# Performance work log

Measured on AMD Instinct MI355X. Metric: run time of the kernel, lower is better.

The kernel has to match this reference:

```python
import jax, jax.numpy as jnp
import numpy as np

NUM_GROUPS = 32
EPS = 1e-05
HT_MIN = -1.0
HT_MAX = 1.0


def setup_inputs() -> dict:
    key = jax.random.key(0)
    k1, k2, k3 = jax.random.split(key, 3)
    B, IN, OUT = 4096, 2048, 2048
    x = jax.random.normal(k1, (B, IN), dtype=jnp.float32)
    # kaiming-uniform-ish scale for weight, uniform bias bound 1/sqrt(in)
    weight = jax.random.normal(k2, (OUT, IN), dtype=jnp.float32) * (1.0 / np.sqrt(IN))
    bias = jax.random.uniform(k3, (OUT,), dtype=jnp.float32, minval=-1.0 / np.sqrt(IN), maxval=1.0 / np.sqrt(IN))
    gn_weight = jnp.ones((OUT,), dtype=jnp.float32)
    gn_bias = jnp.zeros((OUT,), dtype=jnp.float32)
    return {"x": x, "weight": weight, "bias": bias, "gn_weight": gn_weight, "gn_bias": gn_bias}


def reference(x, weight, bias, gn_weight, gn_bias):
    # Linear: y = x @ W^T + b   -> [B, OUT]
    y = jnp.einsum("bi,oi->bo", x, weight) + bias
    B, C = y.shape
    G = NUM_GROUPS
    yg = y.reshape(B, G, C // G)
    mean = jnp.mean(yg, axis=-1, keepdims=True)
    var = jnp.mean(jnp.square(yg), axis=-1, keepdims=True) - jnp.square(mean)
    yn = ((yg - mean) * jax.lax.rsqrt(var + EPS)).reshape(B, C)
    out = yn * gn_weight + gn_bias
    return jnp.clip(out, HT_MIN, HT_MAX)
```

## Files before the change

kernel.cpp:

```cpp
#include <hip/hip_runtime.h>
#include <stdint.h>

#define B_ROWS 4096
#define C_OUT  2048
#define C_IN   2048
#define EPS    1e-5f

typedef __attribute__((ext_vector_type(8))) short bf16x8;
typedef __attribute__((ext_vector_type(4))) float f32x4;

__device__ __forceinline__ unsigned short f2bf(float f) {
    uint32_t u = __float_as_uint(f);
    uint32_t r = (u + 0x7fffu + ((u >> 16) & 1u)) >> 16;
    return (unsigned short)r;
}

__global__ void cvt_f32_bf16_kernel(const float* __restrict__ in,
                                    unsigned short* __restrict__ out, int n4) {
    int i = blockIdx.x * blockDim.x + threadIdx.x;
    if (i < n4) {
        float4 v = ((const float4*)in)[i];
        ushort4 o;
        o.x = f2bf(v.x); o.y = f2bf(v.y); o.z = f2bf(v.z); o.w = f2bf(v.w);
        ((ushort4*)out)[i] = o;
    }
}

__global__ void gemm_gn_kernel(const unsigned short* __restrict__ A,
                               const unsigned short* __restrict__ W,
                               const float* __restrict__ bias,
                               const float* __restrict__ gnw,
                               const float* __restrict__ gnb,
                               float* __restrict__ out) {
    __shared__ unsigned short sA[128 * 32];
    __shared__ unsigned short sB[128 * 32];

    const int bc   = blockIdx.x;
    const int br   = blockIdx.y;
    const int t    = threadIdx.x;
    const int lane = t & 63;
    const int wave = t >> 6;
    const int wr   = wave >> 1;
    const int wc   = wave & 1;
    const int c16  = lane & 15;
    const int quad = lane >> 4;

    f32x4 acc[4][4];
#pragma unroll
    for (int i = 0; i < 4; i++)
#pragma unroll
        for (int j = 0; j < 4; j++) acc[i][j] = (f32x4){0.f, 0.f, 0.f, 0.f};

    const int fl0 = t * 8;
    const int r0  = fl0 >> 5;
    const int kk0 = fl0 & 31;
    const unsigned short* gA = A + (size_t)(br * 128 + r0) * C_IN + kk0;
    const unsigned short* gB = W + (size_t)(bc * 128 + r0) * C_IN + kk0;

    for (int k0 = 0; k0 < C_IN; k0 += 32) {
        __builtin_amdgcn_global_load_lds(
            (const __attribute__((address_space(1))) void*)(gA + k0),
            (__attribute__((address_space(3))) void*)(sA + fl0), 16, 0, 0);
        __builtin_amdgcn_global_load_lds(
            (const __attribute__((address_space(1))) void*)(gA + (size_t)64 * C_IN + k0),
            (__attribute__((address_space(3))) void*)(sA + 2048 + fl0), 16, 0, 0);
        __builtin_amdgcn_global_load_lds(
            (const __attribute__((address_space(1))) void*)(gB + k0),
            (__attribute__((address_space(3))) void*)(sB + fl0), 16, 0, 0);
        __builtin_amdgcn_global_load_lds(
            (const __attribute__((address_space(1))) void*)(gB + (size_t)64 * C_IN + k0),
            (__attribute__((address_space(3))) void*)(sB + 2048 + fl0), 16, 0, 0);
        __syncthreads();

        bf16x8 a[4], b[4];
#pragma unroll
        for (int i = 0; i < 4; i++) {
            a[i] = *(const bf16x8*)(sA + (wr * 64 + i * 16 + c16) * 32 + quad * 8);
            b[i] = *(const bf16x8*)(sB + (wc * 64 + i * 16 + c16) * 32 + quad * 8);
        }
#pragma unroll
        for (int i = 0; i < 4; i++)
#pragma unroll
            for (int j = 0; j < 4; j++)
                acc[i][j] = __builtin_amdgcn_mfma_f32_16x16x32_bf16(a[i], b[j], acc[i][j], 0, 0, 0);
        __syncthreads();
    }

    const int colbase = bc * 128 + wc * 64;
    const int rowbase = br * 128 + wr * 64;
    float bv[4], gw[4], gb[4];
#pragma unroll
    for (int j = 0; j < 4; j++) {
        int col = colbase + j * 16 + c16;
        bv[j] = bias[col];
        gw[j] = gnw[col];
        gb[j] = gnb[col];
    }
#pragma unroll
    for (int i = 0; i < 4; i++) {
#pragma unroll
        for (int r = 0; r < 4; r++) {
            float s = 0.f, ss = 0.f;
#pragma unroll
            for (int j = 0; j < 4; j++) {
                float v = acc[i][j][r] + bv[j];
                acc[i][j][r] = v;
                s += v;
                ss += v * v;
            }
#pragma unroll
            for (int m = 1; m < 16; m <<= 1) {
                s  += __shfl_xor(s, m, 64);
                ss += __shfl_xor(ss, m, 64);
            }
            float mean = s * (1.f / 64.f);
            float var  = ss * (1.f / 64.f) - mean * mean;
            float rstd = rsqrtf(var + EPS);
            int row = rowbase + i * 16 + quad * 4 + r;
            float* orow = out + (size_t)row * C_OUT;
#pragma unroll
            for (int j = 0; j < 4; j++) {
                float v = (acc[i][j][r] - mean) * rstd * gw[j] + gb[j];
                v = fminf(1.f, fmaxf(-1.f, v));
                orow[colbase + j * 16 + c16] = v;
            }
        }
    }
}

extern "C" void kernel_launch(void* const* d_in, const int* in_sizes, int n_in,
                              void* d_out, int out_size, void* d_ws, size_t ws_size,
                              hipStream_t stream) {
    const float* x    = (const float*)d_in[0];
    const float* w    = (const float*)d_in[1];
    const float* bias = (const float*)d_in[2];
    const float* gnw  = (const float*)d_in[3];
    const float* gnb  = (const float*)d_in[4];
    float* out = (float*)d_out;

    unsigned short* xb = (unsigned short*)d_ws;
    unsigned short* wb = xb + (size_t)B_ROWS * C_IN;

    const int nx = B_ROWS * C_IN;
    const int nw = C_OUT * C_IN;
    cvt_f32_bf16_kernel<<<(nx / 4 + 255) / 256, 256, 0, stream>>>(x, xb, nx / 4);
    cvt_f32_bf16_kernel<<<(nw / 4 + 255) / 256, 256, 0, stream>>>(w, wb, nw / 4);

    dim3 grid(C_OUT / 128, B_ROWS / 128);
    gemm_gn_kernel<<<grid, 256, 0, stream>>>(xb, wb, bias, gnw, gnb, out);
}
```

Baseline: 151.8 us.

## Shrink GEMM tile to 128x64, swizzle LDS, merge conversion kernels

New measurement: 159.2 us. +4.8%, slower.

```diff
diff --git a/kernel.cpp b/kernel.cpp
--- a/kernel.cpp
+++ b/kernel.cpp
@@ -15,79 +15,87 @@
     return (unsigned short)r;
 }
 
-__global__ void cvt_f32_bf16_kernel(const float* __restrict__ in,
-                                    unsigned short* __restrict__ out, int n4) {
+__global__ void cvt_f32_bf16_kernel(const float* __restrict__ x,
+                                    const float* __restrict__ w,
+                                    unsigned short* __restrict__ xb,
+                                    unsigned short* __restrict__ wb,
+                                    int nx4, int nw4) {
     int i = blockIdx.x * blockDim.x + threadIdx.x;
-    if (i < n4) {
-        float4 v = ((const float4*)in)[i];
-        ushort4 o;
-        o.x = f2bf(v.x); o.y = f2bf(v.y); o.z = f2bf(v.z); o.w = f2bf(v.w);
-        ((ushort4*)out)[i] = o;
+    const float* src;
+    unsigned short* dst;
+    if (i < nx4) {
+        src = x; dst = xb;
+    } else {
+        i -= nx4;
+        if (i >= nw4) return;
+        src = w; dst = wb;
     }
+    float4 v = ((const float4*)src)[i];
+    ushort4 o;
+    o.x = f2bf(v.x); o.y = f2bf(v.y); o.z = f2bf(v.z); o.w = f2bf(v.w);
+    ((ushort4*)dst)[i] = o;
 }
 
-__global__ void gemm_gn_kernel(const unsigned short* __restrict__ A,
-                               const unsigned short* __restrict__ W,
-                               const float* __restrict__ bias,
-                               const float* __restrict__ gnw,
-                               const float* __restrict__ gnb,
-                               float* __restrict__ out) {
-    __shared__ unsigned short sA[128 * 32];
-    __shared__ unsigned short sB[128 * 32];
+__global__ __launch_bounds__(256, 4)
+void gemm_gn_kernel(const unsigned short* __restrict__ A,
+                    const unsigned short* __restrict__ W,
+                    const float* __restrict__ bias,
+                    const float* __restrict__ gnw,
+                    const float* __restrict__ gnb,
+                    float* __restrict__ out) {
+    __shared__ __align__(16) unsigned short sA[128 * 32];
+    __shared__ __align__(16) unsigned short sB[64 * 32];
 
     const int bc   = blockIdx.x;
     const int br   = blockIdx.y;
     const int t    = threadIdx.x;
     const int lane = t & 63;
     const int wave = t >> 6;
-    const int wr   = wave >> 1;
-    const int wc   = wave & 1;
     const int c16  = lane & 15;
     const int quad = lane >> 4;
 
-    f32x4 acc[4][4];
+    f32x4 acc[2][4];
 #pragma unroll
-    for (int i = 0; i < 4; i++)
+    for (int i = 0; i < 2; i++)
 #pragma unroll
         for (int j = 0; j < 4; j++) acc[i][j] = (f32x4){0.f, 0.f, 0.f, 0.f};
 
-    const int fl0 = t * 8;
-    const int r0  = fl0 >> 5;
-    const int kk0 = fl0 & 31;
-    const unsigned short* gA = A + (size_t)(br * 128 + r0) * C_IN + kk0;
-    const unsigned short* gB = W + (size_t)(bc * 128 + r0) * C_IN + kk0;
+    const int rowA = t >> 2;
+    const int qgA  = (t & 3) ^ ((rowA >> 1) & 3);
+    const unsigned short* gA = A + (size_t)(br * 128 + rowA) * C_IN + qgA * 8;
+    const unsigned short* gB = W + (size_t)(bc * 64 + rowA) * C_IN + qgA * 8;
+
+    const int qs = quad ^ ((c16 >> 1) & 3);
 
     for (int k0 = 0; k0 < C_IN; k0 += 32) {
         __builtin_amdgcn_global_load_lds(
             (const __attribute__((address_space(1))) void*)(gA + k0),
-            (__attribute__((address_space(3))) void*)(sA + fl0), 16, 0, 0);
+            (__attribute__((address_space(3))) void*)(sA + t * 8), 16, 0, 0);
         __builtin_amdgcn_global_load_lds(
             (const __attribute__((address_space(1))) void*)(gA + (size_t)64 * C_IN + k0),
-            (__attribute__((address_space(3))) void*)(sA + 2048 + fl0), 16, 0, 0);
+            (__attribute__((address_space(3))) void*)(sA + 2048 + t * 8), 16, 0, 0);
         __builtin_amdgcn_global_load_lds(
             (const __attribute__((address_space(1))) void*)(gB + k0),
-            (__attribute__((address_space(3))) void*)(sB + fl0), 16, 0, 0);
-        __builtin_amdgcn_global_load_lds(
-            (const __attribute__((address_space(1))) void*)(gB + (size_t)64 * C_IN + k0),
-            (__attribute__((address_space(3))) void*)(sB + 2048 + fl0), 16, 0, 0);
+            (__attribute__((address_space(3))) void*)(sB + t * 8), 16, 0, 0);
         __syncthreads();
 
-        bf16x8 a[4], b[4];
+        bf16x8 a[2], b[4];
 #pragma unroll
-        for (int i = 0; i < 4; i++) {
-            a[i] = *(const bf16x8*)(sA + (wr * 64 + i * 16 + c16) * 32 + quad * 8);
-            b[i] = *(const bf16x8*)(sB + (wc * 64 + i * 16 + c16) * 32 + quad * 8);
-        }
+        for (int i = 0; i < 2; i++)
+            a[i] = *(const bf16x8*)(sA + (wave * 32 + i * 16 + c16) * 32 + qs * 8);
 #pragma unroll
-        for (int i = 0; i < 4; i++)
+        for (int j = 0; j < 4; j++)
+            b[j] = *(const bf16x8*)(sB + (j * 16 + c16) * 32 + qs * 8);
+#pragma unroll
+        for (int i = 0; i < 2; i++)
 #pragma unroll
             for (int j = 0; j < 4; j++)
                 acc[i][j] = __builtin_amdgcn_mfma_f32_16x16x32_bf16(a[i], b[j], acc[i][j], 0, 0, 0);
         __syncthreads();
     }
 
-    const int colbase = bc * 128 + wc * 64;
-    const int rowbase = br * 128 + wr * 64;
+    const int colbase = bc * 64;
+    const int rowbase = br * 128 + wave * 32;
     float bv[4], gw[4], gb[4];
 #pragma unroll
     for (int j = 0; j < 4; j++) {
@@ -97,7 +105,7 @@
         gb[j] = gnb[col];
     }
 #pragma unroll
-    for (int i = 0; i < 4; i++) {
+    for (int i = 0; i < 2; i++) {
 #pragma unroll
         for (int r = 0; r < 4; r++) {
             float s = 0.f, ss = 0.f;
@@ -141,11 +149,10 @@
     unsigned short* xb = (unsigned short*)d_ws;
     unsigned short* wb = xb + (size_t)B_ROWS * C_IN;
 
-    const int nx = B_ROWS * C_IN;
-    const int nw = C_OUT * C_IN;
-    cvt_f32_bf16_kernel<<<(nx / 4 + 255) / 256, 256, 0, stream>>>(x, xb, nx / 4);
-    cvt_f32_bf16_kernel<<<(nw / 4 + 255) / 256, 256, 0, stream>>>(w, wb, nw / 4);
+    const int nx4 = B_ROWS * C_IN / 4;
+    const int nw4 = C_OUT * C_IN / 4;
+    cvt_f32_bf16_kernel<<<(nx4 + nw4 + 255) / 256, 256, 0, stream>>>(x, w, xb, wb, nx4, nw4);
 
-    dim3 grid(C_OUT / 128, B_ROWS / 128);
+    dim3 grid(C_OUT / 64, B_ROWS / 128);
     gemm_gn_kernel<<<grid, 256, 0, stream>>>(xb, wb, bias, gnw, gnb, out);
 }
```
